# Optimization experiments

Measured on AMD Instinct MI355X. Metric: run time of the kernel, lower is better.

The kernel has to match this reference:

```python
import jax, jax.numpy as jnp
import numpy as np

B, L = 4096, 200
USER_COUNT, ITEM_COUNT, CATE_COUNT = 100000, 100000, 1000
USER_DIM, ITEM_DIM, CATE_DIM = 128, 64, 64
BN_EPS = 1e-5


def setup_inputs() -> dict:
    key = jax.random.key(0)
    ks = jax.random.split(key, 16)
    # ragged history: valid prefix of `length` items (ids >= 1), zero-padded tail
    length = jax.random.randint(ks[3], (B,), 1, L + 1)
    hist_raw = jax.random.randint(ks[2], (B, L), 1, ITEM_COUNT)
    history = jnp.where(jnp.arange(L)[None, :] < length[:, None], hist_raw, 0)
    inp = {
        "user": jax.random.randint(ks[0], (B,), 0, USER_COUNT),
        "item": jax.random.randint(ks[1], (B,), 0, ITEM_COUNT),
        "history": history,
        "length": length,
        "cate_list": jax.random.randint(ks[4], (ITEM_COUNT,), 0, CATE_COUNT),
        "user_emb_W": jax.random.normal(ks[5], (USER_COUNT, USER_DIM), jnp.float32) * 0.05,
        "item_emb_W": jax.random.normal(ks[6], (ITEM_COUNT, ITEM_DIM), jnp.float32) * 0.05,
        "cate_emb_W": jax.random.normal(ks[7], (CATE_COUNT, CATE_DIM), jnp.float32) * 0.05,
        "bn_gamma": 1.0 + 0.1 * jax.random.normal(ks[8], (384,), jnp.float32),
        "bn_beta": 0.1 * jax.random.normal(ks[9], (384,), jnp.float32),
        "W1": jax.random.normal(ks[10], (200, 384), jnp.float32) * (1.0 / np.sqrt(384)),
        "b1": jnp.zeros((200,), jnp.float32),
        "a1": jnp.full((), 0.25, jnp.float32),
        "W2": jax.random.normal(ks[11], (80, 200), jnp.float32) * (1.0 / np.sqrt(200)),
        "b2": jnp.zeros((80,), jnp.float32),
        "a2": jnp.full((), 0.25, jnp.float32),
        "W3": jax.random.normal(ks[12], (2, 80), jnp.float32) * (1.0 / np.sqrt(80)),
        "b3": jnp.zeros((2,), jnp.float32),
    }
    return inp


def _prelu(x, a):
    return jnp.where(x >= 0, x, a * x)


def reference(user, item, history, length, cate_list,
              user_emb_W, item_emb_W, cate_emb_W, bn_gamma, bn_beta,
              W1, b1, a1, W2, b2, a2, W3, b3):
    u = user_emb_W[user]                                              # [B,128]
    it = jnp.concatenate([item_emb_W[item], cate_emb_W[cate_list[item]]], -1)  # [B,128]

    # Faithful replication of get_emb's loop semantics:
    # row b uses the prefix of `history[b]` up to (and incl.) the position
    # just before the first zero; a row whose first entry is 0 halts the
    # outer loop, zeroing that row and all following rows.
    nz = history != 0                                                 # [B,L]
    prefix = jnp.concatenate(
        [jnp.ones((history.shape[0], 1), bool),
         jnp.cumprod(nz[:, 1:].astype(jnp.int32), axis=1).astype(bool)], axis=1)
    row_active = jnp.cumprod(nz[:, 0].astype(jnp.int32)).astype(bool)  # outer break
    mask = prefix & row_active[:, None]                               # [B,L]

    he = jnp.concatenate([item_emb_W[history], cate_emb_W[cate_list[history]]], -1)  # [B,L,128]
    cnt = jnp.maximum(mask.sum(-1), 1).astype(he.dtype)               # [B]
    pooled = (he * mask[..., None].astype(he.dtype)).sum(1) / cnt[:, None]  # [B,128]

    x = jnp.concatenate([u, it, pooled], -1)                          # [B,384]
    # BatchNorm1d in training mode (batch stats, biased variance)
    mean = x.mean(0)
    var = x.var(0)
    x = (x - mean) * jax.lax.rsqrt(var + BN_EPS) * bn_gamma + bn_beta
    x = _prelu(x @ W1.T + b1, a1)
    x = _prelu(x @ W2.T + b2, a2)
    x = x @ W3.T + b3
    return jax.nn.softmax(x, axis=1)
```

## Files before the change

### kernel.cpp

```cpp
#include <hip/hip_runtime.h>
#include <hip/hip_bf16.h>

#define B_SZ 4096
#define L_SZ 200

typedef __bf16 bf16x8 __attribute__((ext_vector_type(8)));
typedef float  f32x4  __attribute__((ext_vector_type(4)));

static __device__ inline unsigned short bfbits(float f) {
    return __builtin_bit_cast(unsigned short, (__bf16)f);
}
static __device__ inline float bf2f(unsigned short u) {
    return __builtin_bit_cast(float, (unsigned int)u << 16);
}

__global__ __launch_bounds__(64) void k_wfrag(const float* __restrict__ W1,
                                              const float* __restrict__ W2,
                                              ushort* __restrict__ W1f,
                                              ushort* __restrict__ W2f,
                                              const int* __restrict__ history,
                                              int* __restrict__ first_bad) {
    const int bid = blockIdx.x, lane = threadIdx.x;
    if (bid >= 191) {
        const int base = (bid - 191) * 512 + lane;
        int m = 0x7f7f7f7f;
        #pragma unroll
        for (int i = 0; i < 8; ++i) {
            int b = base + i * 64;
            if (history[(size_t)b * L_SZ] == 0) m = min(m, b);
        }
        if (m != 0x7f7f7f7f) atomicMin(first_bad, m);
        return;
    }
    const int nr = lane & 15, quad = lane >> 4;
    ushort v[8];
    if (bid < 156) {
        const int oT = bid / 12, kS = bid % 12;
        const int o = oT * 16 + nr;
        #pragma unroll
        for (int j = 0; j < 8; ++j) {
            int k = kS * 32 + quad * 8 + j;
            v[j] = (o < 200) ? bfbits(W1[(size_t)o * 384 + k]) : (ushort)0;
        }
        ushort* dst = W1f + ((size_t)bid * 64 + lane) * 8;
        *(ushort4*)(dst)     = make_ushort4(v[0], v[1], v[2], v[3]);
        *(ushort4*)(dst + 4) = make_ushort4(v[4], v[5], v[6], v[7]);
    } else {
        const int idx = bid - 156;
        const int oT = idx / 7, kS = idx % 7;
        const int o = oT * 16 + nr;
        #pragma unroll
        for (int j = 0; j < 8; ++j) {
            int k = kS * 32 + quad * 8 + j;
            v[j] = (k < 200) ? bfbits(W2[(size_t)o * 200 + k]) : (ushort)0;
        }
        ushort* dst = W2f + ((size_t)idx * 64 + lane) * 8;
        *(ushort4*)(dst)     = make_ushort4(v[0], v[1], v[2], v[3]);
        *(ushort4*)(dst + 4) = make_ushort4(v[4], v[5], v[6], v[7]);
    }
}

__global__ __launch_bounds__(256) void k_pool(
    const int* __restrict__ user, const int* __restrict__ item,
    const int* __restrict__ history, const int* __restrict__ cate_list,
    const float* __restrict__ user_W, const float* __restrict__ item_W,
    const float* __restrict__ cate_W, const int* __restrict__ first_bad,
    ushort* __restrict__ xb)
{
    const int b = blockIdx.x;
    const int tid = threadIdx.x;
    __shared__ int sh_item[L_SZ];
    __shared__ int sh_cid[L_SZ];
    __shared__ int s_fz;
    __shared__ __align__(16) float red[8][128];
    if (tid == 0) s_fz = L_SZ;
    __syncthreads();
    if (tid < L_SZ) {
        int h = history[(size_t)b * L_SZ + tid];
        sh_item[tid] = h;
        if (tid >= 1 && h == 0) atomicMin(&s_fz, tid);
        sh_cid[tid] = cate_list[h];
    }
    __syncthreads();
    const bool active = (b < first_bad[0]);
    const int valid = active ? s_fz : 0;
    const float inv_cnt = 1.0f / (float)max(valid, 1);

    const int group = tid >> 5, lane = tid & 31;
    const int sub = lane >> 4, q = lane & 15;
    const float* tab = (sub == 0) ? item_W : cate_W;
    const int*   ids = (sub == 0) ? sh_item : sh_cid;
    float4 acc = make_float4(0.f, 0.f, 0.f, 0.f);
    int l = group;
    for (; l + 8 < valid; l += 16) {
        int id0 = ids[l], id1 = ids[l + 8];
        float4 v0 = ((const float4*)(tab + (size_t)id0 * 64))[q];
        float4 v1 = ((const float4*)(tab + (size_t)id1 * 64))[q];
        acc.x += v0.x + v1.x; acc.y += v0.y + v1.y;
        acc.z += v0.z + v1.z; acc.w += v0.w + v1.w;
    }
    if (l < valid) {
        int id = ids[l];
        float4 v = ((const float4*)(tab + (size_t)id * 64))[q];
        acc.x += v.x; acc.y += v.y; acc.z += v.z; acc.w += v.w;
    }
    *((float4*)&red[group][lane * 4]) = acc;
    __syncthreads();

    ushort* xrow = xb + (size_t)b * 384;
    if (tid < 128) {
        float s = 0.f;
        #pragma unroll
        for (int g = 0; g < 8; ++g) s += red[g][tid];
        xrow[256 + tid] = bfbits(s * inv_cnt);
        xrow[tid] = bfbits(user_W[(size_t)user[b] * 128 + tid]);
    } else if (tid < 192) {
        int f = tid - 128;
        xrow[128 + f] = bfbits(item_W[(size_t)item[b] * 64 + f]);
    } else {
        int f = tid - 192;
        xrow[192 + f] = bfbits(cate_W[(size_t)cate_list[item[b]] * 64 + f]);
    }
}

__global__ __launch_bounds__(384) void k_bnstats(const ushort* __restrict__ xb,
                                                 float* __restrict__ acc) {
    const int f = threadIdx.x;
    const int r0 = blockIdx.x * 16;
    float s = 0.f, s2 = 0.f;
    for (int r = r0; r < r0 + 16; ++r) {
        float v = bf2f(xb[(size_t)r * 384 + f]);
        s += v; s2 += v * v;
    }
    atomicAdd(&acc[f], s);
    atomicAdd(&acc[384 + f], s2);
}

__global__ __launch_bounds__(256) void k_l1(
    const ushort* __restrict__ xb, const float* __restrict__ accv,
    const float* __restrict__ gamma, const float* __restrict__ beta,
    const ushort* __restrict__ W1f, const float* __restrict__ b1,
    const float* __restrict__ a1p, ushort* __restrict__ h1b)
{
    __shared__ float As[384], Cs[384];
    const int tid = threadIdx.x;
    for (int f = tid; f < 384; f += 256) {
        const float inv_b = 1.0f / (float)B_SZ;
        float mean = accv[f] * inv_b;
        float var  = accv[384 + f] * inv_b - mean * mean;
        float a = gamma[f] * rsqrtf(var + 1e-5f);
        As[f] = a;
        Cs[f] = beta[f] - mean * a;
    }
    __syncthreads();

    const int lane = tid & 63, wv = tid >> 6;
    const int nr = lane & 15, quad = lane >> 4;
    const int wid = blockIdx.x * 4 + wv;
    const int mT = wid / 13, oT = wid - mT * 13;
    const int o = oT * 16 + nr;
    const float a1 = a1p[0];

    float bias = (o < 200) ? b1[o] : 0.f;
    f32x4 acc = {bias, bias, bias, bias};
    const ushort* xrow = xb + (size_t)(mT * 16 + nr) * 384;

    for (int kS = 0; kS < 12; ++kS) {
        const int kc = kS * 32 + quad * 8;
        bf16x8 a8 = *(const bf16x8*)(xrow + kc);
        float4 A0 = *(const float4*)&As[kc],     A1 = *(const float4*)&As[kc + 4];
        float4 C0 = *(const float4*)&Cs[kc],     C1 = *(const float4*)&Cs[kc + 4];
        bf16x8 w;
        w[0] = (__bf16)((float)a8[0] * A0.x + C0.x);
        w[1] = (__bf16)((float)a8[1] * A0.y + C0.y);
        w[2] = (__bf16)((float)a8[2] * A0.z + C0.z);
        w[3] = (__bf16)((float)a8[3] * A0.w + C0.w);
        w[4] = (__bf16)((float)a8[4] * A1.x + C1.x);
        w[5] = (__bf16)((float)a8[5] * A1.y + C1.y);
        w[6] = (__bf16)((float)a8[6] * A1.z + C1.z);
        w[7] = (__bf16)((float)a8[7] * A1.w + C1.w);
        bf16x8 bfr = *(const bf16x8*)(W1f + (((size_t)oT * 12 + kS) * 64 + lane) * 8);
        acc = __builtin_amdgcn_mfma_f32_16x16x32_bf16(w, bfr, acc, 0, 0, 0);
    }

    #pragma unroll
    for (int r = 0; r < 4; ++r) {
        int row = mT * 16 + quad * 4 + r;
        float s = acc[r];
        s = (s >= 0.f) ? s : a1 * s;
        h1b[(size_t)row * 224 + o] = bfbits(s);
        if (oT == 12) h1b[(size_t)row * 224 + o + 16] = 0;
    }
}

__global__ __launch_bounds__(64) void k_l23(
    const ushort* __restrict__ h1b, const ushort* __restrict__ W2f,
    const float* __restrict__ b2, const float* __restrict__ a2p,
    const float* __restrict__ W3, const float* __restrict__ b3,
    float* __restrict__ out)
{
    const int lane = threadIdx.x;
    const int nr = lane & 15, quad = lane >> 4;
    const int mT = blockIdx.x;
    const float a2 = a2p[0];

    f32x4 acc[5];
    #pragma unroll
    for (int i = 0; i < 5; ++i) {
        float bb = b2[i * 16 + nr];
        acc[i] = (f32x4){bb, bb, bb, bb};
    }
    const ushort* hrow = h1b + (size_t)(mT * 16 + nr) * 224;
    for (int kS = 0; kS < 7; ++kS) {
        bf16x8 a8 = *(const bf16x8*)(hrow + kS * 32 + quad * 8);
        #pragma unroll
        for (int i = 0; i < 5; ++i) {
            bf16x8 bfr = *(const bf16x8*)(W2f + (((size_t)i * 7 + kS) * 64 + lane) * 8);
            acc[i] = __builtin_amdgcn_mfma_f32_16x16x32_bf16(a8, bfr, acc[i], 0, 0, 0);
        }
    }

    float w0[5], w1[5];
    #pragma unroll
    for (int i = 0; i < 5; ++i) {
        w0[i] = W3[i * 16 + nr];
        w1[i] = W3[80 + i * 16 + nr];
    }
    f32x4 p0 = {0.f, 0.f, 0.f, 0.f}, p1 = {0.f, 0.f, 0.f, 0.f};
    #pragma unroll
    for (int i = 0; i < 5; ++i) {
        #pragma unroll
        for (int r = 0; r < 4; ++r) {
            float s = acc[i][r];
            s = (s >= 0.f) ? s : a2 * s;
            p0[r] += s * w0[i];
            p1[r] += s * w1[i];
        }
    }
    #pragma unroll
    for (int m = 1; m < 16; m <<= 1) {
        #pragma unroll
        for (int r = 0; r < 4; ++r) {
            p0[r] += __shfl_xor(p0[r], m, 64);
            p1[r] += __shfl_xor(p1[r], m, 64);
        }
    }
    if (nr == 0) {
        float B0 = b3[0], B1 = b3[1];
        #pragma unroll
        for (int r = 0; r < 4; ++r) {
            float l0 = p0[r] + B0, l1 = p1[r] + B1;
            float mx = fmaxf(l0, l1);
            float e0 = expf(l0 - mx), e1 = expf(l1 - mx);
            float inv = 1.0f / (e0 + e1);
            int row = mT * 16 + quad * 4 + r;
            *(float2*)(out + (size_t)row * 2) = make_float2(e0 * inv, e1 * inv);
        }
    }
}

extern "C" void kernel_launch(void* const* d_in, const int* in_sizes, int n_in,
                              void* d_out, int out_size, void* d_ws, size_t ws_size,
                              hipStream_t stream) {
    const int*   user      = (const int*)  d_in[0];
    const int*   item      = (const int*)  d_in[1];
    const int*   history   = (const int*)  d_in[2];
    const int*   cate_list = (const int*)  d_in[4];
    const float* user_W    = (const float*)d_in[5];
    const float* item_W    = (const float*)d_in[6];
    const float* cate_W    = (const float*)d_in[7];
    const float* gamma     = (const float*)d_in[8];
    const float* beta      = (const float*)d_in[9];
    const float* W1        = (const float*)d_in[10];
    const float* b1        = (const float*)d_in[11];
    const float* a1        = (const float*)d_in[12];
    const float* W2        = (const float*)d_in[13];
    const float* b2        = (const float*)d_in[14];
    const float* a2        = (const float*)d_in[15];
    const float* W3        = (const float*)d_in[16];
    const float* b3        = (const float*)d_in[17];
    float* out = (float*)d_out;

    char* ws = (char*)d_ws;
    int*    first_bad = (int*)   ws;
    float*  acc       = (float*)(ws + 64);
    ushort* xb        = (ushort*)(ws + 3200);
    ushort* h1b       = (ushort*)(ws + 3148928);
    ushort* W1f       = (ushort*)(ws + 4983936);
    ushort* W2f       = (ushort*)(ws + 5143680);

    hipMemsetAsync(first_bad, 0x7F, 4, stream);
    hipMemsetAsync(acc, 0, 768 * sizeof(float), stream);

    hipLaunchKernelGGL(k_wfrag,   dim3(199),  dim3(64),   0, stream,
                       W1, W2, W1f, W2f, history, first_bad);
    hipLaunchKernelGGL(k_pool,    dim3(B_SZ), dim3(256),  0, stream,
                       user, item, history, cate_list, user_W, item_W, cate_W,
                       first_bad, xb);
    hipLaunchKernelGGL(k_bnstats, dim3(256),  dim3(384),  0, stream, xb, acc);
    hipLaunchKernelGGL(k_l1,      dim3(832),  dim3(256),  0, stream,
                       xb, acc, gamma, beta, W1f, b1, a1, h1b);
    hipLaunchKernelGGL(k_l23,     dim3(256),  dim3(64),   0, stream,
                       h1b, W2f, b2, a2, W3, b3, out);
}
```

Baseline: 177.5 us.

## Pre-convert embedding tables to bf16, fuse MLP layers, and merge setup kernels

A new prep kernel converts the full item and category embedding tables to bf16 on every call. It also builds the W1/W2 MFMA fragments, computes first_bad with a block reduction, and zeroes the BN accumulators, which removes the two memsets. The pooling kernel then gathers half-width bf16 rows, aiming to cut history-gather traffic. Layers 1–3 are fused into one 832-thread block per 16-row tile, with h1 kept in shared memory instead of a global round trip. The trade-off is a full-table read and write each call (about 25.6MB read, 12.8MB written), and a single wave doing layers 2–3 while the other twelve sit idle.

Result: no change. 179.4 us (+1.1%).

```diff
diff --git a/kernel.cpp b/kernel.cpp
--- a/kernel.cpp
+++ b/kernel.cpp
@@ -3,6 +3,8 @@
 
 #define B_SZ 4096
 #define L_SZ 200
+#define ITEM_ELEMS 6400000
+#define CATE_ELEMS 64000
 
 typedef __bf16 bf16x8 __attribute__((ext_vector_type(8)));
 typedef float  f32x4  __attribute__((ext_vector_type(4)));
@@ -14,57 +16,98 @@
     return __builtin_bit_cast(float, (unsigned int)u << 16);
 }
 
-__global__ __launch_bounds__(64) void k_wfrag(const float* __restrict__ W1,
-                                              const float* __restrict__ W2,
-                                              ushort* __restrict__ W1f,
-                                              ushort* __restrict__ W2f,
-                                              const int* __restrict__ history,
-                                              int* __restrict__ first_bad) {
-    const int bid = blockIdx.x, lane = threadIdx.x;
-    if (bid >= 191) {
-        const int base = (bid - 191) * 512 + lane;
-        int m = 0x7f7f7f7f;
-        #pragma unroll
-        for (int i = 0; i < 8; ++i) {
-            int b = base + i * 64;
+__global__ __launch_bounds__(256) void k_prep(
+    const float* __restrict__ W1, const float* __restrict__ W2,
+    ushort* __restrict__ W1f, ushort* __restrict__ W2f,
+    const int* __restrict__ history, int* __restrict__ first_bad,
+    float* __restrict__ acc,
+    const float* __restrict__ item_W, const float* __restrict__ cate_W,
+    ushort* __restrict__ item_bf, ushort* __restrict__ cate_bf)
+{
+    const int bid = blockIdx.x, tid = threadIdx.x;
+
+    if (bid < 48) {
+        const int lane = tid & 63, wv = tid >> 6;
+        const int t = bid * 4 + wv;
+        if (t >= 191) return;
+        const int nr = lane & 15, quad = lane >> 4;
+        ushort v[8];
+        if (t < 156) {
+            const int oT = t / 12, kS = t - oT * 12;
+            const int o = oT * 16 + nr;
+            #pragma unroll
+            for (int j = 0; j < 8; ++j) {
+                int k = kS * 32 + quad * 8 + j;
+                v[j] = (o < 200) ? bfbits(W1[(size_t)o * 384 + k]) : (ushort)0;
+            }
+            ushort* dst = W1f + ((size_t)t * 64 + lane) * 8;
+            *(ushort4*)(dst)     = make_ushort4(v[0], v[1], v[2], v[3]);
+            *(ushort4*)(dst + 4) = make_ushort4(v[4], v[5], v[6], v[7]);
+        } else {
+            const int idx = t - 156;
+            const int oT = idx / 7, kS = idx - oT * 7;
+            const int o = oT * 16 + nr;
+            #pragma unroll
+            for (int j = 0; j < 8; ++j) {
+                int k = kS * 32 + quad * 8 + j;
+                v[j] = (k < 200) ? bfbits(W2[(size_t)o * 200 + k]) : (ushort)0;
+            }
+            ushort* dst = W2f + ((size_t)idx * 64 + lane) * 8;
+            *(ushort4*)(dst)     = make_ushort4(v[0], v[1], v[2], v[3]);
+            *(ushort4*)(dst + 4) = make_ushort4(v[4], v[5], v[6], v[7]);
+        }
+        return;
+    }
+
+    if (bid == 48) {
+        acc[tid] = 0.f; acc[256 + tid] = 0.f; acc[512 + tid] = 0.f;
+        int m = B_SZ;
+        #pragma unroll
+        for (int i = 0; i < 16; ++i) {
+            int b = tid + i * 256;
             if (history[(size_t)b * L_SZ] == 0) m = min(m, b);
         }
-        if (m != 0x7f7f7f7f) atomicMin(first_bad, m);
+        __shared__ int red[256];
+        red[tid] = m;
+        __syncthreads();
+        for (int s = 128; s > 0; s >>= 1) {
+            if (tid < s) red[tid] = min(red[tid], red[tid + s]);
+            __syncthreads();
+        }
+        if (tid == 0) first_bad[0] = red[0];
         return;
     }
-    const int nr = lane & 15, quad = lane >> 4;
-    ushort v[8];
-    if (bid < 156) {
-        const int oT = bid / 12, kS = bid % 12;
-        const int o = oT * 16 + nr;
-        #pragma unroll
-        for (int j = 0; j < 8; ++j) {
-            int k = kS * 32 + quad * 8 + j;
-            v[j] = (o < 200) ? bfbits(W1[(size_t)o * 384 + k]) : (ushort)0;
-        }
-        ushort* dst = W1f + ((size_t)bid * 64 + lane) * 8;
-        *(ushort4*)(dst)     = make_ushort4(v[0], v[1], v[2], v[3]);
-        *(ushort4*)(dst + 4) = make_ushort4(v[4], v[5], v[6], v[7]);
-    } else {
-        const int idx = bid - 156;
-        const int oT = idx / 7, kS = idx % 7;
-        const int o = oT * 16 + nr;
-        #pragma unroll
-        for (int j = 0; j < 8; ++j) {
-            int k = kS * 32 + quad * 8 + j;
-            v[j] = (k < 200) ? bfbits(W2[(size_t)o * 200 + k]) : (ushort)0;
-        }
-        ushort* dst = W2f + ((size_t)idx * 64 + lane) * 8;
-        *(ushort4*)(dst)     = make_ushort4(v[0], v[1], v[2], v[3]);
-        *(ushort4*)(dst + 4) = make_ushort4(v[4], v[5], v[6], v[7]);
+
+    if (bid == 49) {
+        for (int i = tid * 8; i < CATE_ELEMS; i += 256 * 8) {
+            float4 a = *(const float4*)(cate_W + i);
+            float4 b = *(const float4*)(cate_W + i + 4);
+            *(ushort4*)(cate_bf + i) =
+                make_ushort4(bfbits(a.x), bfbits(a.y), bfbits(a.z), bfbits(a.w));
+            *(ushort4*)(cate_bf + i + 4) =
+                make_ushort4(bfbits(b.x), bfbits(b.y), bfbits(b.z), bfbits(b.w));
+        }
+        return;
+    }
+
+    {
+        const size_t step = (size_t)(gridDim.x - 50) * 256 * 8;
+        for (size_t i = ((size_t)(bid - 50) * 256 + tid) * 8; i < ITEM_ELEMS; i += step) {
+            float4 a = *(const float4*)(item_W + i);
+            float4 b = *(const float4*)(item_W + i + 4);
+            *(ushort4*)(item_bf + i) =
+                make_ushort4(bfbits(a.x), bfbits(a.y), bfbits(a.z), bfbits(a.w));
+            *(ushort4*)(item_bf + i + 4) =
+                make_ushort4(bfbits(b.x), bfbits(b.y), bfbits(b.z), bfbits(b.w));
+        }
     }
 }
 
 __global__ __launch_bounds__(256) void k_pool(
     const int* __restrict__ user, const int* __restrict__ item,
     const int* __restrict__ history, const int* __restrict__ cate_list,
-    const float* __restrict__ user_W, const float* __restrict__ item_W,
-    const float* __restrict__ cate_W, const int* __restrict__ first_bad,
+    const float* __restrict__ user_W, const ushort* __restrict__ item_bf,
+    const ushort* __restrict__ cate_bf, const int* __restrict__ first_bad,
     ushort* __restrict__ xb)
 {
     const int b = blockIdx.x;
@@ -88,21 +131,24 @@
 
     const int group = tid >> 5, lane = tid & 31;
     const int sub = lane >> 4, q = lane & 15;
-    const float* tab = (sub == 0) ? item_W : cate_W;
-    const int*   ids = (sub == 0) ? sh_item : sh_cid;
+    const ushort* tab = (sub == 0) ? item_bf : cate_bf;
+    const int*    ids = (sub == 0) ? sh_item : sh_cid;
     float4 acc = make_float4(0.f, 0.f, 0.f, 0.f);
     int l = group;
     for (; l + 8 < valid; l += 16) {
         int id0 = ids[l], id1 = ids[l + 8];
-        float4 v0 = ((const float4*)(tab + (size_t)id0 * 64))[q];
-        float4 v1 = ((const float4*)(tab + (size_t)id1 * 64))[q];
-        acc.x += v0.x + v1.x; acc.y += v0.y + v1.y;
-        acc.z += v0.z + v1.z; acc.w += v0.w + v1.w;
+        ushort4 v0 = ((const ushort4*)(tab + (size_t)id0 * 64))[q];
+        ushort4 v1 = ((const ushort4*)(tab + (size_t)id1 * 64))[q];
+        acc.x += bf2f(v0.x) + bf2f(v1.x);
+        acc.y += bf2f(v0.y) + bf2f(v1.y);
+        acc.z += bf2f(v0.z) + bf2f(v1.z);
+        acc.w += bf2f(v0.w) + bf2f(v1.w);
     }
     if (l < valid) {
         int id = ids[l];
-        float4 v = ((const float4*)(tab + (size_t)id * 64))[q];
-        acc.x += v.x; acc.y += v.y; acc.z += v.z; acc.w += v.w;
+        ushort4 v = ((const ushort4*)(tab + (size_t)id * 64))[q];
+        acc.x += bf2f(v.x); acc.y += bf2f(v.y);
+        acc.z += bf2f(v.z); acc.w += bf2f(v.w);
     }
     *((float4*)&red[group][lane * 4]) = acc;
     __syncthreads();
@@ -116,10 +162,10 @@
         xrow[tid] = bfbits(user_W[(size_t)user[b] * 128 + tid]);
     } else if (tid < 192) {
         int f = tid - 128;
-        xrow[128 + f] = bfbits(item_W[(size_t)item[b] * 64 + f]);
+        xrow[128 + f] = item_bf[(size_t)item[b] * 64 + f];
     } else {
         int f = tid - 192;
-        xrow[192 + f] = bfbits(cate_W[(size_t)cate_list[item[b]] * 64 + f]);
+        xrow[192 + f] = cate_bf[(size_t)cate_list[item[b]] * 64 + f];
     }
 }
 
@@ -136,28 +182,32 @@
     atomicAdd(&acc[384 + f], s2);
 }
 
-__global__ __launch_bounds__(256) void k_l1(
+__global__ __launch_bounds__(832) void k_l123(
     const ushort* __restrict__ xb, const float* __restrict__ accv,
     const float* __restrict__ gamma, const float* __restrict__ beta,
     const ushort* __restrict__ W1f, const float* __restrict__ b1,
-    const float* __restrict__ a1p, ushort* __restrict__ h1b)
+    const float* __restrict__ a1p, const ushort* __restrict__ W2f,
+    const float* __restrict__ b2, const float* __restrict__ a2p,
+    const float* __restrict__ W3, const float* __restrict__ b3,
+    float* __restrict__ out)
 {
     __shared__ float As[384], Cs[384];
+    __shared__ __align__(16) ushort h1s[16][232];
     const int tid = threadIdx.x;
-    for (int f = tid; f < 384; f += 256) {
+    if (tid < 384) {
         const float inv_b = 1.0f / (float)B_SZ;
-        float mean = accv[f] * inv_b;
-        float var  = accv[384 + f] * inv_b - mean * mean;
-        float a = gamma[f] * rsqrtf(var + 1e-5f);
-        As[f] = a;
-        Cs[f] = beta[f] - mean * a;
+        float mean = accv[tid] * inv_b;
+        float var  = accv[384 + tid] * inv_b - mean * mean;
+        float a = gamma[tid] * rsqrtf(var + 1e-5f);
+        As[tid] = a;
+        Cs[tid] = beta[tid] - mean * a;
     }
     __syncthreads();
 
     const int lane = tid & 63, wv = tid >> 6;
     const int nr = lane & 15, quad = lane >> 4;
-    const int wid = blockIdx.x * 4 + wv;
-    const int mT = wid / 13, oT = wid - mT * 13;
+    const int mT = blockIdx.x;
+    const int oT = wv;
     const int o = oT * 16 + nr;
     const float a1 = a1p[0];
 
@@ -185,38 +235,29 @@
 
     #pragma unroll
     for (int r = 0; r < 4; ++r) {
-        int row = mT * 16 + quad * 4 + r;
+        int row = quad * 4 + r;
         float s = acc[r];
         s = (s >= 0.f) ? s : a1 * s;
-        h1b[(size_t)row * 224 + o] = bfbits(s);
-        if (oT == 12) h1b[(size_t)row * 224 + o + 16] = 0;
-    }
-}
-
-__global__ __launch_bounds__(64) void k_l23(
-    const ushort* __restrict__ h1b, const ushort* __restrict__ W2f,
-    const float* __restrict__ b2, const float* __restrict__ a2p,
-    const float* __restrict__ W3, const float* __restrict__ b3,
-    float* __restrict__ out)
-{
-    const int lane = threadIdx.x;
-    const int nr = lane & 15, quad = lane >> 4;
-    const int mT = blockIdx.x;
+        h1s[row][o] = bfbits(s);
+        if (oT == 12) h1s[row][o + 16] = 0;
+    }
+    __syncthreads();
+
+    if (wv != 0) return;
+
     const float a2 = a2p[0];
-
-    f32x4 acc[5];
+    f32x4 acc2[5];
     #pragma unroll
     for (int i = 0; i < 5; ++i) {
         float bb = b2[i * 16 + nr];
-        acc[i] = (f32x4){bb, bb, bb, bb};
-    }
-    const ushort* hrow = h1b + (size_t)(mT * 16 + nr) * 224;
+        acc2[i] = (f32x4){bb, bb, bb, bb};
+    }
     for (int kS = 0; kS < 7; ++kS) {
-        bf16x8 a8 = *(const bf16x8*)(hrow + kS * 32 + quad * 8);
+        bf16x8 a8 = *(const bf16x8*)(&h1s[nr][kS * 32 + quad * 8]);
         #pragma unroll
         for (int i = 0; i < 5; ++i) {
             bf16x8 bfr = *(const bf16x8*)(W2f + (((size_t)i * 7 + kS) * 64 + lane) * 8);
-            acc[i] = __builtin_amdgcn_mfma_f32_16x16x32_bf16(a8, bfr, acc[i], 0, 0, 0);
+            acc2[i] = __builtin_amdgcn_mfma_f32_16x16x32_bf16(a8, bfr, acc2[i], 0, 0, 0);
         }
     }
 
@@ -231,7 +272,7 @@
     for (int i = 0; i < 5; ++i) {
         #pragma unroll
         for (int r = 0; r < 4; ++r) {
-            float s = acc[i][r];
+            float s = acc2[i][r];
             s = (s >= 0.f) ? s : a2 * s;
             p0[r] += s * w0[i];
             p1[r] += s * w1[i];
@@ -285,21 +326,18 @@
     int*    first_bad = (int*)   ws;
     float*  acc       = (float*)(ws + 64);
     ushort* xb        = (ushort*)(ws + 3200);
-    ushort* h1b       = (ushort*)(ws + 3148928);
-    ushort* W1f       = (ushort*)(ws + 4983936);
-    ushort* W2f       = (ushort*)(ws + 5143680);
-
-    hipMemsetAsync(first_bad, 0x7F, 4, stream);
-    hipMemsetAsync(acc, 0, 768 * sizeof(float), stream);
-
-    hipLaunchKernelGGL(k_wfrag,   dim3(199),  dim3(64),   0, stream,
-                       W1, W2, W1f, W2f, history, first_bad);
-    hipLaunchKernelGGL(k_pool,    dim3(B_SZ), dim3(256),  0, stream,
-                       user, item, history, cate_list, user_W, item_W, cate_W,
+    ushort* W1f       = (ushort*)(ws + 3148928);
+    ushort* W2f       = (ushort*)(ws + 3308672);
+    ushort* cate_bf   = (ushort*)(ws + 3344512);
+    ushort* item_bf   = (ushort*)(ws + 3472512);
+
+    hipLaunchKernelGGL(k_prep,    dim3(1074), dim3(256), 0, stream,
+                       W1, W2, W1f, W2f, history, first_bad, acc,
+                       item_W, cate_W, item_bf, cate_bf);
+    hipLaunchKernelGGL(k_pool,    dim3(B_SZ), dim3(256), 0, stream,
+                       user, item, history, cate_list, user_W, item_bf, cate_bf,
                        first_bad, xb);
-    hipLaunchKernelGGL(k_bnstats, dim3(256),  dim3(384),  0, stream, xb, acc);
-    hipLaunchKernelGGL(k_l1,      dim3(832),  dim3(256),  0, stream,
-                       xb, acc, gamma, beta, W1f, b1, a1, h1b);
-    hipLaunchKernelGGL(k_l23,     dim3(256),  dim3(64),   0, stream,
-                       h1b, W2f, b2, a2, W3, b3, out);
-}
+    hipLaunchKernelGGL(k_bnstats, dim3(256),  dim3(384), 0, stream, xb, acc);
+    hipLaunchKernelGGL(k_l123,    dim3(256),  dim3(832), 0, stream,
+                       xb, acc, gamma, beta, W1f, b1, a1, W2f, b2, a2, W3, b3, out);
+}
```
